# Performance work log

Measured on AMD Instinct MI355X. Metric: run time of the kernel, lower is better.

## Reference

```python
import jax, jax.numpy as jnp
import numpy as np

B, T = 64, 500
N_EX, N_SK = 10000, 100
H, K = 128, 32


def setup_inputs() -> dict:
    key = jax.random.key(0)
    ks = jax.random.split(key, 32)
    g = lambda i, shape, s=0.05: (jax.random.normal(ks[i], shape, dtype=jnp.float32) * s)
    inp = {
        's_data': jax.random.randint(ks[0], (B, T), 0, N_SK),
        'a_data': jax.random.randint(ks[1], (B, T), 0, 2),
        'e_data': jax.random.randint(ks[2], (B, T), 0, N_EX),
        'at_data': jax.random.randint(ks[3], (B, T), 0, 100),
        'q_matrix': (jax.random.uniform(ks[4], (N_EX + 1, N_SK + 1)) < 0.05).astype(jnp.float32),
        's_embed_w': g(5, (N_SK + 1, H)),
        'a_embed_w': g(6, (2, H)),
        'e_embed_w': g(7, (N_EX + 1, H)),
        'W1': g(8, (H, 2 * H)), 'b1': jnp.zeros((H,), jnp.float32),
        'W2': g(9, (H, 3 * H)), 'b2': jnp.zeros((H,), jnp.float32),
        'W3': g(10, (H, 2 * H)), 'b3': jnp.zeros((H,), jnp.float32),
        'key_matrix': g(11, (K, H)),
        'gru_w_ih': g(12, (3 * H, H)), 'gru_w_hh': g(13, (3 * H, H)),
        'gru_b_ih': jnp.zeros((3 * H,), jnp.float32), 'gru_b_hh': jnp.zeros((3 * H,), jnp.float32),
        'Wg': g(14, (H, 2 * H)), 'bg': jnp.zeros((H,), jnp.float32),
        'Wgg': g(15, (H, 2 * H)), 'bgg': jnp.zeros((H,), jnp.float32),
        'Wf': g(16, (H, 2 * H)), 'bf': jnp.zeros((H,), jnp.float32),
        'Wp': g(17, (1, 3 * H)), 'bp': jnp.zeros((1,), jnp.float32),
        'Wp1': g(18, (1, 3 * H)), 'bp1': jnp.zeros((1,), jnp.float32),
        'h0': g(19, (H,)),           # xavier init of GRU initial state (shared across batch)
        'm0': g(20, (K, H)),         # xavier init of memory h_pre (shared across batch)
    }
    return inp


def reference(s_data, a_data, e_data, at_data, q_matrix, s_embed_w, a_embed_w, e_embed_w,
              W1, b1, W2, b2, W3, b3, key_matrix, gru_w_ih, gru_w_hh, gru_b_ih, gru_b_hh,
              Wg, bg, Wgg, bgg, Wf, bf, Wp, bp, Wp1, bp1, h0, m0):
    # eval mode: dropout = identity
    Bv, Tv = a_data.shape
    lin = lambda x, W, b: x @ W.T + b
    # ---- embedding (n_exercise > 0 branch) ----
    rel = q_matrix[e_data]                              # [B,T,S+1]
    ssum = rel.sum(-1, keepdims=True)
    ssum = jnp.where(ssum == 0, 1.0, ssum)
    s_emb = jnp.einsum('bts,sh->bth', rel, s_embed_w) / ssum
    e_emb = e_embed_w[e_data]
    a_emb = a_embed_w[a_data]
    se_data = jax.nn.relu(lin(jnp.concatenate([s_emb, e_emb], -1), W1, b1))
    se_learning = jax.nn.relu(lin(jnp.concatenate([s_emb, e_emb, a_emb], -1), W2, b2))
    e_learning = jax.nn.relu(lin(jnp.concatenate([e_emb, a_emb], -1), W3, b3))
    # ---- GRU over e_learning ----
    gx = jnp.einsum('bth,gh->btg', e_learning, gru_w_ih) + gru_b_ih  # [B,T,3H]
    def gru_step(h, gxt):
        gh = h @ gru_w_hh.T + gru_b_hh
        xr, xz, xn = jnp.split(gxt, 3, -1)
        hr, hz, hn = jnp.split(gh, 3, -1)
        r = jax.nn.sigmoid(xr + hr)
        z = jax.nn.sigmoid(xz + hz)
        n = jnp.tanh(xn + r * hn)
        hn2 = (1 - z) * n + z * h
        return hn2, hn2
    _, gru_out = jax.lax.scan(gru_step, jnp.broadcast_to(h0, (Bv, h0.shape[0])), jnp.swapaxes(gx, 0, 1))
    out = jnp.swapaxes(gru_out, 0, 1)[:, :-1]           # [B,T-1,H]
    # ---- key-value memory scan ----
    Wall = jnp.einsum('bth,kh->btk', se_data, key_matrix)  # attention weights (unnormalized)
    h_pre0 = jnp.broadcast_to(m0, (Bv,) + m0.shape)        # [B,K,H]
    ht0 = jnp.einsum('bk,bkh->bh', Wall[:, 0], h_pre0)
    xs = (jnp.swapaxes(Wall[:, :-1], 0, 1),
          jnp.swapaxes(Wall[:, 1:], 0, 1),
          jnp.swapaxes(se_learning[:, :-1], 0, 1))
    def step(carry, x):
        h_pre, ht_pre = carry
        w, w_next, learning = x
        hl = jnp.concatenate([ht_pre, learning], -1)
        gain = jnp.tanh(hl @ Wg.T + bg)
        gate = jax.nn.sigmoid(hl @ Wgg.T + bgg)
        LG = gate * gain                                  # [B,H]
        LG_t = w[:, :, None] * LG[:, None, :]             # [B,K,H] write
        gam = jax.nn.sigmoid(jnp.concatenate([h_pre, jnp.broadcast_to(LG[:, None, :], h_pre.shape)], -1) @ Wf.T + bf)
        h = gam * h_pre + LG_t
        ht = jnp.einsum('bk,bkh->bh', w_next, h)          # read at t+1
        return (h, ht), ht
    _, hts = jax.lax.scan(step, (h_pre0, ht0), xs)
    out1 = jnp.swapaxes(hts, 0, 1)                        # [B,T-1,H]
    sg = jax.lax.stop_gradient
    res = jax.nn.sigmoid(jnp.concatenate([out, sg(out1), e_emb[:, 1:]], -1) @ Wp.T + bp)[..., 0]
    res1 = jax.nn.sigmoid(jnp.concatenate([sg(out), out1, se_data[:, 1:]], -1) @ Wp1.T + bp1)[..., 0]
    pred = jnp.zeros((Bv, Tv), res.dtype).at[:, 1:].set(res * res1)
    return pred
```

## Files before the change

### kernel.cpp

```cpp
#include <hip/hip_runtime.h>

#define TT 500
typedef __attribute__((ext_vector_type(8))) short short8v;
typedef __attribute__((ext_vector_type(4))) short short4v;
typedef __attribute__((ext_vector_type(4))) float float4v;
typedef unsigned short ushort;

__device__ __forceinline__ ushort f2bf(float f) {
  union { float f; unsigned u; } v; v.f = f;
  unsigned r = v.u + 0x7FFFu + ((v.u >> 16) & 1u);
  return (ushort)(r >> 16);
}
__device__ __forceinline__ ushort f2bfr(float f) {
  union { float f; unsigned u; } v; v.f = f;
  return (ushort)((v.u + 0x8000u) >> 16);
}
__device__ __forceinline__ float bf2f(ushort u) {
  union { unsigned u; float f; } v; v.u = ((unsigned)u) << 16;
  return v.f;
}
__device__ __forceinline__ float sigm(float x) {
  return __builtin_amdgcn_rcpf(1.f + __builtin_amdgcn_exp2f(-1.44269504088896341f * x));
}
__device__ __forceinline__ float tanh_f(float x) {
  return 1.f - 2.f * __builtin_amdgcn_rcpf(1.f + __builtin_amdgcn_exp2f(2.88539008177792682f * x));
}
__device__ __forceinline__ void bar_lds() {
  asm volatile("s_waitcnt lgkmcnt(0)\ns_barrier" ::: "memory");
}
template <int CTRL>
__device__ __forceinline__ float dppadd(float v) {
  int a = __builtin_amdgcn_update_dpp(0, __builtin_bit_cast(int, v), CTRL, 0xF, 0xF, true);
  return v + __builtin_bit_cast(float, a);
}
__device__ __forceinline__ float rsum16(float v) {
  v = dppadd<0xB1>(v);
  v = dppadd<0x4E>(v);
  v = dppadd<0x141>(v);
  v = dppadd<0x140>(v);
  return v;
}
__device__ __forceinline__ void wait_flag(int* f) {
  while (__hip_atomic_load(f, __ATOMIC_RELAXED, __HIP_MEMORY_SCOPE_AGENT) == 0)
    __builtin_amdgcn_s_sleep(8);
  __builtin_amdgcn_fence(__ATOMIC_ACQUIRE, "agent");
}
#define MFMA __builtin_amdgcn_mfma_f32_16x16x32_bf16

__global__ __launch_bounds__(256) void conv_k(
    const float* __restrict__ W1, const float* __restrict__ W2,
    const float* __restrict__ W3, const float* __restrict__ Wih,
    const float* __restrict__ key, const float* __restrict__ Wg,
    const float* __restrict__ Wgg, ushort* __restrict__ wts)
{
  int idx = blockIdx.x * 256 + threadIdx.x;
  if (idx >= 200704) return;
  float v;
  if (idx < 32768)       v = W1[idx];
  else if (idx < 81920)  v = W2[idx - 32768];
  else if (idx < 114688) v = W3[idx - 81920];
  else if (idx < 163840) v = Wih[idx - 114688];
  else if (idx < 167936) v = key[idx - 163840];
  else {
    int j = idx - 167936, o = j >> 7, k = j & 127;
    v = (o < 128) ? Wg[o * 256 + 128 + k] : Wgg[(o - 128) * 256 + 128 + k];
  }
  wts[idx] = f2bf(v);
}

#define XS 424
#define SS 648

__global__ __launch_bounds__(512, 2) void mega_k(
    const int* __restrict__ a_data, const int* __restrict__ e_data,
    const float* __restrict__ qm, const float* __restrict__ semb,
    const float* __restrict__ aemb, const float* __restrict__ eemb,
    const float* __restrict__ b1, const float* __restrict__ b2,
    const float* __restrict__ b3, const float* __restrict__ bih,
    const float* __restrict__ bg, const float* __restrict__ bgg,
    const float* __restrict__ Wp, const float* __restrict__ bp,
    const float* __restrict__ Wp1, const float* __restrict__ bp1,
    const ushort* __restrict__ wts,
    const float* __restrict__ Wf, const float* __restrict__ bf_,
    const float* __restrict__ Wg, const float* __restrict__ Wgg,
    const float* __restrict__ Whh, const float* __restrict__ bhh,
    const float* __restrict__ h0v, const float* __restrict__ m0,
    ushort* __restrict__ gxb, ushort* __restrict__ xgx,
    float* __restrict__ wallb, float* __restrict__ c1b, float* __restrict__ c2b,
    ushort* __restrict__ htsm, ushort* __restrict__ htsg,
    int* __restrict__ flags)
{
  __shared__ __align__(16) ushort pool[27136];
  const int tid = threadIdx.x;
  const int w = tid >> 6, l = tid & 63, jj = l & 15, seg = l >> 4;
  const int n0 = w * 16 + seg * 4;

  if (blockIdx.x < 64) {
    __builtin_amdgcn_s_setprio(3);
    const int b = blockIdx.x;
    ushort* h_bf = pool;
    ushort* htb  = pool + 4096;
    ushort* LGb  = pool + 4224;

    short8v afrA[4], aggA[4], aggB[4], alg[4];
#pragma unroll
    for (int ks = 0; ks < 4; ++ks) {
      const float* sA = Wf  + (w * 16 + jj) * 256 + ks * 32 + seg * 8;
      const float* sB = Wg  + (w * 16 + jj) * 256 + ks * 32 + seg * 8;
      const float* sC = Wgg + (w * 16 + jj) * 256 + ks * 32 + seg * 8;
      const float* sD = Wf  + (w * 16 + jj) * 256 + 128 + ks * 32 + seg * 8;
      short8v a, bb, c, d;
#pragma unroll
      for (int j = 0; j < 8; ++j) {
        a[j] = (short)f2bf(sA[j]); bb[j] = (short)f2bf(sB[j]);
        c[j] = (short)f2bf(sC[j]); d[j] = (short)f2bf(sD[j]);
      }
      afrA[ks] = a; aggA[ks] = bb; aggB[ks] = c; alg[ks] = d;
    }
    const float4v bf4 = *(const float4v*)(bf_ + n0);

    float hreg[2][4];
#pragma unroll
    for (int nt = 0; nt < 2; ++nt) {
      int k = nt * 16 + jj;
      float4v m = *(const float4v*)(m0 + k * 128 + n0);
#pragma unroll
      for (int r = 0; r < 4; ++r) hreg[nt][r] = m[r];
      int p = ((n0 >> 3) + k) & 15;
      short4v pk;
#pragma unroll
      for (int r = 0; r < 4; ++r) pk[r] = (short)f2bf(hreg[nt][r]);
      *(short4v*)(h_bf + k * 128 + p * 8 + (n0 & 7)) = pk;
    }
    wait_flag(flags + b);
    const float* wl = wallb + (size_t)b * TT * 32;
    const ushort* xgp = xgx + (size_t)b * TT * 256;
    float wv0 = wl[jj], wv1 = wl[16 + jj];
    float wn0 = wl[32 + jj], wn1 = wl[48 + jj];
    short4v xcg  = *(const short4v*)(xgp + n0);
    short4v xcgg = *(const short4v*)(xgp + 128 + n0);
    short4v xng  = *(const short4v*)(xgp + 256 + n0);
    short4v xngg = *(const short4v*)(xgp + 384 + n0);
    {
      float4v htp;
#pragma unroll
      for (int r = 0; r < 4; ++r)
        htp[r] = rsum16(wv0 * hreg[0][r] + wv1 * hreg[1][r]);
      if (jj == 0) {
        short4v hp;
#pragma unroll
        for (int r = 0; r < 4; ++r) hp[r] = (short)f2bf(htp[r]);
        *(short4v*)(htb + n0) = hp;
      }
    }
    __syncthreads();

    for (int t = 0; t < TT - 1; ++t) {
      int tw = (t + 2 <= TT - 1) ? (t + 2) : (TT - 1);
      if ((tw & 31) == 0) wait_flag(flags + (tw >> 5) * 64 + b);
      float wf0 = wl[tw * 32 + jj], wf1 = wl[tw * 32 + 16 + jj];
      short4v xfg  = *(const short4v*)(xgp + (size_t)tw * 256 + n0);
      short4v xfgg = *(const short4v*)(xgp + (size_t)tw * 256 + 128 + n0);

      short8v hb[4];
#pragma unroll
      for (int ks = 0; ks < 4; ++ks)
        hb[ks] = *(short8v*)(htb + ks * 32 + seg * 8);

      float4v xg4, xgg4;
#pragma unroll
      for (int r = 0; r < 4; ++r) { xg4[r] = bf2f((ushort)xcg[r]); xgg4[r] = bf2f((ushort)xcgg[r]); }
      float4v dg0 = xg4, dg1 = {0,0,0,0}, gg0 = xgg4, gg1 = {0,0,0,0};
      dg0 = MFMA(aggA[0], hb[0], dg0, 0, 0, 0);
      dg0 = MFMA(aggA[1], hb[1], dg0, 0, 0, 0);
      dg1 = MFMA(aggA[2], hb[2], dg1, 0, 0, 0);
      dg1 = MFMA(aggA[3], hb[3], dg1, 0, 0, 0);
      gg0 = MFMA(aggB[0], hb[0], gg0, 0, 0, 0);
      gg0 = MFMA(aggB[1], hb[1], gg0, 0, 0, 0);
      gg1 = MFMA(aggB[2], hb[2], gg1, 0, 0, 0);
      gg1 = MFMA(aggB[3], hb[3], gg1, 0, 0, 0);

      float lgv[4];
#pragma unroll
      for (int r = 0; r < 4; ++r)
        lgv[r] = tanh_f(dg0[r] + dg1[r]) * sigm(gg0[r] + gg1[r]);
      if (jj == 0) {
        short4v lp;
#pragma unroll
        for (int r = 0; r < 4; ++r) lp[r] = (short)f2bfr(lgv[r]);
        *(short4v*)(LGb + n0) = lp;
      }

      short8v bv0[4], bv1[4];
#pragma unroll
      for (int ks = 0; ks < 4; ++ks) {
        int g = ks * 4 + seg;
        bv0[ks] = *(short8v*)(h_bf + jj * 128 + ((g + jj) & 15) * 8);
        bv1[ks] = *(short8v*)(h_bf + (16 + jj) * 128 + ((g + 16 + jj) & 15) * 8);
      }
      float4v a0A = {0,0,0,0}, a0B = {0,0,0,0}, a1A = {0,0,0,0}, a1B = {0,0,0,0};
      a0A = MFMA(afrA[0], bv0[0], a0A, 0, 0, 0);
      a0A = MFMA(afrA[1], bv0[1], a0A, 0, 0, 0);
      a0B = MFMA(afrA[2], bv0[2], a0B, 0, 0, 0);
      a0B = MFMA(afrA[3], bv0[3], a0B, 0, 0, 0);
      a1A = MFMA(afrA[0], bv1[0], a1A, 0, 0, 0);
      a1A = MFMA(afrA[1], bv1[1], a1A, 0, 0, 0);
      a1B = MFMA(afrA[2], bv1[2], a1B, 0, 0, 0);
      a1B = MFMA(afrA[3], bv1[3], a1B, 0, 0, 0);
      bar_lds();

      short8v lb[4];
#pragma unroll
      for (int ks = 0; ks < 4; ++ks)
        lb[ks] = *(short8v*)(LGb + ks * 32 + seg * 8);
      float4v dl0 = bf4, dl1 = {0,0,0,0};
      dl0 = MFMA(alg[0], lb[0], dl0, 0, 0, 0);
      dl0 = MFMA(alg[1], lb[1], dl0, 0, 0, 0);
      dl1 = MFMA(alg[2], lb[2], dl1, 0, 0, 0);
      dl1 = MFMA(alg[3], lb[3], dl1, 0, 0, 0);

      float4v htp = {0,0,0,0};
#pragma unroll
      for (int nt = 0; nt < 2; ++nt) {
        float wvv = nt ? wv1 : wv0;
        float wnn = nt ? wn1 : wn0;
#pragma unroll
        for (int r = 0; r < 4; ++r) {
          float a = nt ? (a1A[r] + a1B[r]) : (a0A[r] + a0B[r]);
          float gam = sigm(a + dl0[r] + dl1[r]);
          float hn = fmaf(gam, hreg[nt][r], wvv * lgv[r]);
          hreg[nt][r] = hn;
          htp[r] = fmaf(wnn, hn, htp[r]);
        }
        int k = nt * 16 + jj;
        int p = ((n0 >> 3) + k) & 15;
        short4v pk;
#pragma unroll
        for (int r = 0; r < 4; ++r) pk[r] = (short)f2bfr(hreg[nt][r]);
        *(short4v*)(h_bf + k * 128 + p * 8 + (n0 & 7)) = pk;
      }
#pragma unroll
      for (int r = 0; r < 4; ++r) htp[r] = rsum16(htp[r]);
      if (jj == 0) {
        short4v hp;
#pragma unroll
        for (int r = 0; r < 4; ++r) hp[r] = (short)f2bfr(htp[r]);
        *(short4v*)(htb + n0) = hp;
        *(short4v*)(htsm + ((size_t)b * TT + t) * 128 + n0) = hp;
      }
      wv0 = wn0; wv1 = wn1; wn0 = wf0; wn1 = wf1;
      xcg = xng; xcgg = xngg; xng = xfg; xngg = xfgg;
      bar_lds();
    }
  } else if (blockIdx.x < 128) {
    __builtin_amdgcn_s_setprio(3);
    const int b = blockIdx.x - 64;
    ushort* hb2 = pool;

    short8v wfr[3][4];
    float4v bfr[3];
#pragma unroll
    for (int i = 0; i < 3; ++i) {
      int Mt = w + i * 8;
#pragma unroll
      for (int ks = 0; ks < 4; ++ks) {
        const float* src = Whh + (Mt * 16 + jj) * 128 + ks * 32 + seg * 8;
        short8v tv;
#pragma unroll
        for (int j = 0; j < 8; ++j) tv[j] = (short)f2bf(src[j]);
        wfr[i][ks] = tv;
      }
      bfr[i] = *(const float4v*)(bhh + Mt * 16 + seg * 4);
    }
    float4v hj4 = *(const float4v*)(h0v + n0);
    if (jj == 0) {
      short4v hp;
#pragma unroll
      for (int r = 0; r < 4; ++r) hp[r] = (short)f2bf(hj4[r]);
      *(short4v*)(hb2 + n0) = hp;
    }
    wait_flag(flags + b);
    const ushort* gpb = gxb + (size_t)b * TT * 384;
    short4v xr_c = *(const short4v*)(gpb + n0);
    short4v xz_c = *(const short4v*)(gpb + 128 + n0);
    short4v xn_c = *(const short4v*)(gpb + 256 + n0);
    short4v xr_n = *(const short4v*)(gpb + 384 + n0);
    short4v xz_n = *(const short4v*)(gpb + 512 + n0);
    short4v xn_n = *(const short4v*)(gpb + 640 + n0);
    __syncthreads();

    for (int t = 0; t < TT - 1; ++t) {
      int tf = (t + 2 < TT - 1) ? (t + 2) : (TT - 2);
      if ((tf & 31) == 0) wait_flag(flags + (tf >> 5) * 64 + b);
      const ushort* gf = gpb + (size_t)tf * 384;
      short4v xr_f = *(const short4v*)(gf + n0);
      short4v xz_f = *(const short4v*)(gf + 128 + n0);
      short4v xn_f = *(const short4v*)(gf + 256 + n0);

      const ushort* hsrc = hb2 + (t & 1) * 128;
      short8v bfrg[4];
#pragma unroll
      for (int ks = 0; ks < 4; ++ks)
        bfrg[ks] = *(short8v*)(hsrc + ks * 32 + seg * 8);

      float4v a0A = bfr[0], a1A = bfr[1], a2A = bfr[2];
      float4v a0B = {0,0,0,0}, a1B = {0,0,0,0}, a2B = {0,0,0,0};
      a0A = MFMA(wfr[0][0], bfrg[0], a0A, 0, 0, 0);
      a0A = MFMA(wfr[0][1], bfrg[1], a0A, 0, 0, 0);
      a0B = MFMA(wfr[0][2], bfrg[2], a0B, 0, 0, 0);
      a0B = MFMA(wfr[0][3], bfrg[3], a0B, 0, 0, 0);
      a1A = MFMA(wfr[1][0], bfrg[0], a1A, 0, 0, 0);
      a1A = MFMA(wfr[1][1], bfrg[1], a1A, 0, 0, 0);
      a1B = MFMA(wfr[1][2], bfrg[2], a1B, 0, 0, 0);
      a1B = MFMA(wfr[1][3], bfrg[3], a1B, 0, 0, 0);
      a2A = MFMA(wfr[2][0], bfrg[0], a2A, 0, 0, 0);
      a2A = MFMA(wfr[2][1], bfrg[1], a2A, 0, 0, 0);
      a2B = MFMA(wfr[2][2], bfrg[2], a2B, 0, 0, 0);
      a2B = MFMA(wfr[2][3], bfrg[3], a2B, 0, 0, 0);

      ushort* hdst = hb2 + ((t + 1) & 1) * 128;
      short4v hp;
#pragma unroll
      for (int r = 0; r < 4; ++r) {
        float rr = sigm(bf2f((ushort)xr_c[r]) + a0A[r] + a0B[r]);
        float zz = sigm(bf2f((ushort)xz_c[r]) + a1A[r] + a1B[r]);
        float nn = tanh_f(bf2f((ushort)xn_c[r]) + rr * (a2A[r] + a2B[r]));
        hj4[r] = fmaf(1.f - zz, nn, zz * hj4[r]);
        hp[r] = (short)f2bfr(hj4[r]);
      }
      if (jj == 0) {
        *(short4v*)(hdst + n0) = hp;
        *(short4v*)(htsg + ((size_t)b * TT + t) * 128 + n0) = hp;
      }
      xr_c = xr_n; xz_c = xz_n; xn_c = xn_n;
      xr_n = xr_f; xz_n = xz_f; xn_n = xn_f;
      bar_lds();
    }
  } else {
    __builtin_amdgcn_s_setprio(0);
    const int gi = blockIdx.x - 128;
    const int chunk = gi >> 6, b = gi & 63;
    const int t0 = chunk * 32;
    const int NT = (TT - t0 < 32) ? (TT - t0) : 32;
    ushort* Xl = pool;
    ushort* Yl = pool + 13568;
    ushort* St = pool;
    const ushort* w1b  = wts;
    const ushort* w2b  = wts + 32768;
    const ushort* w3b  = wts + 81920;
    const ushort* wihb = wts + 114688;
    const ushort* keyb = wts + 163840;
    const ushort* wgb  = wts + 167936;

    {
      const int tok = tid >> 4, l16 = tid & 15;
      const int tsrc = (tok < NT) ? tok : (NT - 1);
      const int gt = b * TT + t0 + tsrc;
      const int e = e_data[gt], a = a_data[gt];
      const float* qrow = qm + (size_t)e * 101;
      float qv[7];
#pragma unroll
      for (int i = 0; i < 7; ++i) {
        int s = l16 + 16 * i;
        qv[i] = (s < 101) ? qrow[s] : 0.f;
      }
      const float* sbase = semb + l16 * 8;
      float4v acc0 = {0,0,0,0}, acc1 = {0,0,0,0};
      float cnt = 0.f;
#pragma unroll
      for (int i = 0; i < 7; ++i) {
        unsigned long long bal = __ballot(qv[i] != 0.f);
        unsigned m = (unsigned)((bal >> (tid & 48)) & 0xFFFFull);
        cnt += (float)__popc(m);
        while (m) {
          int s = 16 * i + __builtin_ctz(m);
          m &= m - 1;
          acc0 += *(const float4v*)(sbase + s * 128);
          acc1 += *(const float4v*)(sbase + s * 128 + 4);
        }
      }
      float inv = 1.f / fmaxf(cnt, 1.f);
      ushort* xr = Xl + tok * XS + l16 * 8;
#pragma unroll
      for (int r = 0; r < 4; ++r) { xr[r] = f2bf(acc0[r] * inv); xr[4 + r] = f2bf(acc1[r] * inv); }
      const float* ee = eemb + (size_t)e * 128 + l16 * 8;
      const float* ae = aemb + a * 128 + l16 * 8;
#pragma unroll
      for (int r = 0; r < 8; ++r) { xr[128 + r] = f2bf(ee[r]); xr[256 + r] = f2bf(ae[r]); }
    }
    __syncthreads();

    if (tid < 32) {
      int tau = tid;
      if (tau < NT) {
        const ushort* xr = Xl + tau * XS + 128;
        const float* wv = Wp + 256;
        float a0 = bp[0], a1 = 0.f, a2 = 0.f, a3 = 0.f;
        for (int j = 0; j < 128; j += 4) {
          a0 = fmaf(wv[j],     bf2f(xr[j]),     a0);
          a1 = fmaf(wv[j + 1], bf2f(xr[j + 1]), a1);
          a2 = fmaf(wv[j + 2], bf2f(xr[j + 2]), a2);
          a3 = fmaf(wv[j + 3], bf2f(xr[j + 3]), a3);
        }
        c1b[b * TT + t0 + tau] = (a0 + a1) + (a2 + a3);
      }
    }

    short8v axA[12], axB[12];
#pragma unroll
    for (int i = 0; i < 12; ++i) {
      axA[i] = *(short8v*)(Xl + jj * XS + i * 32 + seg * 8);
      axB[i] = *(short8v*)(Xl + (16 + jj) * XS + i * 32 + seg * 8);
    }

    for (int T = w; T < 24; T += 8) {
      float4v dA = {0,0,0,0}, dB = {0,0,0,0};
      float bv;
      if (T < 8) {
        const ushort* Bp = w1b + (T * 16 + jj) * 256 + seg * 8;
        bv = b1[T * 16 + jj];
#pragma unroll
        for (int k = 0; k < 8; ++k) {
          short8v bw = *(const short8v*)(Bp + k * 32);
          dA = MFMA(axA[k], bw, dA, 0, 0, 0);
          dB = MFMA(axB[k], bw, dB, 0, 0, 0);
        }
      } else if (T < 16) {
        const ushort* Bp = w2b + ((T - 8) * 16 + jj) * 384 + seg * 8;
        bv = b2[(T - 8) * 16 + jj];
#pragma unroll
        for (int k = 0; k < 12; ++k) {
          short8v bw = *(const short8v*)(Bp + k * 32);
          dA = MFMA(axA[k], bw, dA, 0, 0, 0);
          dB = MFMA(axB[k], bw, dB, 0, 0, 0);
        }
      } else {
        const ushort* Bp = w3b + ((T - 16) * 16 + jj) * 256 + seg * 8;
        bv = b3[(T - 16) * 16 + jj];
#pragma unroll
        for (int k = 0; k < 8; ++k) {
          short8v bw = *(const short8v*)(Bp + k * 32);
          dA = MFMA(axA[4 + k], bw, dA, 0, 0, 0);
          dB = MFMA(axB[4 + k], bw, dB, 0, 0, 0);
        }
      }
#pragma unroll
      for (int r = 0; r < 4; ++r) {
        float yA = dA[r] + bv, yB = dB[r] + bv;
        Yl[(seg * 4 + r) * XS + T * 16 + jj]      = f2bf(yA > 0.f ? yA : 0.f);
        Yl[(16 + seg * 4 + r) * XS + T * 16 + jj] = f2bf(yB > 0.f ? yB : 0.f);
      }
    }
    __syncthreads();

    short8v ayA[12], ayB[12];
#pragma unroll
    for (int i = 0; i < 12; ++i) {
      ayA[i] = *(short8v*)(Yl + jj * XS + i * 32 + seg * 8);
      ayB[i] = *(short8v*)(Yl + (16 + jj) * XS + i * 32 + seg * 8);
    }
    if (tid >= 32 && tid < 64) {
      int tau = tid - 32;
      if (tau < NT) {
        const ushort* xr = Yl + tau * XS;
        const float* wv = Wp1 + 256;
        float a0 = bp1[0], a1 = 0.f, a2 = 0.f, a3 = 0.f;
        for (int j = 0; j < 128; j += 4) {
          a0 = fmaf(wv[j],     bf2f(xr[j]),     a0);
          a1 = fmaf(wv[j + 1], bf2f(xr[j + 1]), a1);
          a2 = fmaf(wv[j + 2], bf2f(xr[j + 2]), a2);
          a3 = fmaf(wv[j + 3], bf2f(xr[j + 3]), a3);
        }
        c2b[b * TT + t0 + tau] = (a0 + a1) + (a2 + a3);
      }
    }
    __syncthreads();

    for (int T = w; T < 42; T += 8) {
      const ushort* Bp; int ai;
      if (T < 24)      { Bp = wihb + (T * 16 + jj) * 128 + seg * 8;        ai = 8; }
      else if (T < 40) { Bp = wgb  + ((T - 24) * 16 + jj) * 128 + seg * 8; ai = 4; }
      else             { Bp = keyb + ((T - 40) * 16 + jj) * 128 + seg * 8; ai = 0; }
      float4v dA = {0,0,0,0}, dB = {0,0,0,0};
#pragma unroll
      for (int k = 0; k < 4; ++k) {
        short8v bw = *(const short8v*)(Bp + k * 32);
        dA = MFMA(ayA[ai + k], bw, dA, 0, 0, 0);
        dB = MFMA(ayB[ai + k], bw, dB, 0, 0, 0);
      }
      if (T < 40) {
        float bv = (T < 24) ? bih[T * 16 + jj]
                 : (T < 32) ? bg[(T - 24) * 16 + jj] : bgg[(T - 32) * 16 + jj];
        int col = (T < 24) ? (T * 16 + jj) : (384 + (T - 24) * 16 + jj);
#pragma unroll
        for (int r = 0; r < 4; ++r) {
          St[(seg * 4 + r) * SS + col]      = f2bf(dA[r] + bv);
          St[(16 + seg * 4 + r) * SS + col] = f2bf(dB[r] + bv);
        }
      } else {
#pragma unroll
        for (int r = 0; r < 4; ++r) {
          int tokA = seg * 4 + r, tokB = 16 + seg * 4 + r;
          if (tokA < NT)
            wallb[((size_t)(b * TT + t0 + tokA)) * 32 + (T - 40) * 16 + jj] = dA[r];
          if (tokB < NT)
            wallb[((size_t)(b * TT + t0 + tokB)) * 32 + (T - 40) * 16 + jj] = dB[r];
        }
      }
    }
    __syncthreads();

    {
      const int tok = tid >> 4, sg = tid & 15;
      if (tok < NT) {
        size_t gt = (size_t)b * TT + t0 + tok;
#pragma unroll
        for (int p = 0; p < 3; ++p)
          *(short8v*)(gxb + gt * 384 + sg * 24 + p * 8) = *(short8v*)(St + tok * SS + sg * 24 + p * 8);
#pragma unroll
        for (int p = 0; p < 2; ++p)
          *(short8v*)(xgx + gt * 256 + sg * 16 + p * 8) = *(short8v*)(St + tok * SS + 384 + sg * 16 + p * 8);
      }
    }
    __syncthreads();
    if (tid == 0)
      __hip_atomic_store(flags + chunk * 64 + b, 1, __ATOMIC_RELEASE, __HIP_MEMORY_SCOPE_AGENT);
  }
}

__global__ __launch_bounds__(256) void combine_k(
    const ushort* __restrict__ htsg, const ushort* __restrict__ htsm,
    const float* __restrict__ c1b, const float* __restrict__ c2b,
    const float* __restrict__ Wp, const float* __restrict__ Wp1,
    float* __restrict__ out)
{
  const int b = blockIdx.x >> 2, q = blockIdx.x & 3;
  const int tid = threadIdx.x;
  const int wv = tid >> 6, l = tid & 63, slot = l >> 4, e = l & 15;
  float wpg[8], wpm[8], vpg[8], vpm[8];
#pragma unroll
  for (int r = 0; r < 8; ++r) {
    wpg[r] = Wp[e * 8 + r];  wpm[r] = Wp[128 + e * 8 + r];
    vpg[r] = Wp1[e * 8 + r]; vpm[r] = Wp1[128 + e * 8 + r];
  }
  if (q == 0 && tid == 0) out[(size_t)b * TT] = 0.f;
  const int tbeg = q * 125;
  const int tend = (tbeg + 125 < TT - 1) ? (tbeg + 125) : (TT - 1);
  for (int tau = tbeg + wv * 4 + slot; tau < tend; tau += 16) {
    size_t base = ((size_t)b * TT + tau) * 128;
    short8v hg = *(const short8v*)(htsg + base + e * 8);
    short8v hm = *(const short8v*)(htsm + base + e * 8);
    float qa = 0.f, qb = 0.f;
#pragma unroll
    for (int r = 0; r < 8; ++r) {
      float g = bf2f((ushort)hg[r]), m = bf2f((ushort)hm[r]);
      qa = fmaf(g, wpg[r], fmaf(m, wpm[r], qa));
      qb = fmaf(g, vpg[r], fmaf(m, vpm[r], qb));
    }
    qa = rsum16(qa);
    qb = rsum16(qb);
    if (e == 0) {
      size_t idx = (size_t)b * TT + tau + 1;
      out[idx] = sigm(qa + c1b[idx]) * sigm(qb + c2b[idx]);
    }
  }
}

extern "C" void kernel_launch(void* const* d_in, const int* in_sizes, int n_in,
                              void* d_out, int out_size, void* d_ws, size_t ws_size,
                              hipStream_t stream) {
  (void)in_sizes; (void)n_in; (void)out_size; (void)ws_size;
  const int* a_data = (const int*)d_in[1];
  const int* e_data = (const int*)d_in[2];
  const float* qm   = (const float*)d_in[4];
  const float* semb = (const float*)d_in[5];
  const float* aemb = (const float*)d_in[6];
  const float* eemb = (const float*)d_in[7];
  const float* W1 = (const float*)d_in[8];   const float* b1 = (const float*)d_in[9];
  const float* W2 = (const float*)d_in[10];  const float* b2 = (const float*)d_in[11];
  const float* W3 = (const float*)d_in[12];  const float* b3 = (const float*)d_in[13];
  const float* key = (const float*)d_in[14];
  const float* Wih = (const float*)d_in[15]; const float* Whh = (const float*)d_in[16];
  const float* bih = (const float*)d_in[17]; const float* bhh = (const float*)d_in[18];
  const float* Wg  = (const float*)d_in[19]; const float* bg  = (const float*)d_in[20];
  const float* Wgg = (const float*)d_in[21]; const float* bgg = (const float*)d_in[22];
  const float* Wf  = (const float*)d_in[23]; const float* bf_ = (const float*)d_in[24];
  const float* Wp  = (const float*)d_in[25]; const float* bp  = (const float*)d_in[26];
  const float* Wp1 = (const float*)d_in[27]; const float* bp1 = (const float*)d_in[28];
  const float* h0v = (const float*)d_in[29]; const float* m0  = (const float*)d_in[30];

  char* ws = (char*)d_ws;
  ushort* gxb  = (ushort*)(ws + 0);
  ushort* xgx  = (ushort*)(ws + 24576000);
  float* wallb = (float*)(ws + 40960000);
  ushort* htsm = (ushort*)(ws + 45056000);
  ushort* htsg = (ushort*)(ws + 53248000);
  float* c1b   = (float*)(ws + 61440000);
  float* c2b   = (float*)(ws + 61568000);
  ushort* wts  = (ushort*)(ws + 61696000);
  int* flags   = (int*)(ws + 62097408);
  float* out = (float*)d_out;

  hipMemsetAsync(flags, 0, 1024 * sizeof(int), stream);
  conv_k<<<dim3(784), dim3(256), 0, stream>>>(W1, W2, W3, Wih, key, Wg, Wgg, wts);
  mega_k<<<dim3(1152), dim3(512), 0, stream>>>(
      a_data, e_data, qm, semb, aemb, eemb, b1, b2, b3, bih, bg, bgg,
      Wp, bp, Wp1, bp1, wts, Wf, bf_, Wg, Wgg, Whh, bhh, h0v, m0,
      gxb, xgx, wallb, c1b, c2b, htsm, htsg, flags);
  combine_k<<<dim3(256), dim3(256), 0, stream>>>(
      htsg, htsm, c1b, c2b, Wp, Wp1, out);
}
```

Baseline: 833.4 us.

## Split memory-recurrence block into gain-gate warps and forget-gate warps

The per-batch memory-update block is split by role. Four waves compute the LG gain/gate MFMAs and publish LG through LDS in both bf16 and fp32. The other four waves compute the Wf forget-gate MFMAs against the memory state and do the state update, each wave covering twice as many columns. The aim is to overlap the LG computation with the h_pre matmul, but each wave now does double work per step and the LG result crosses an LDS barrier. This changes the critical-path length of the serial recurrence.

```diff
diff --git a/kernel.cpp b/kernel.cpp
--- a/kernel.cpp
+++ b/kernel.cpp
@@ -101,156 +101,222 @@
     ushort* h_bf = pool;
     ushort* htb  = pool + 4096;
     ushort* LGb  = pool + 4224;
-
-    short8v afrA[4], aggA[4], aggB[4], alg[4];
-#pragma unroll
-    for (int ks = 0; ks < 4; ++ks) {
-      const float* sA = Wf  + (w * 16 + jj) * 256 + ks * 32 + seg * 8;
-      const float* sB = Wg  + (w * 16 + jj) * 256 + ks * 32 + seg * 8;
-      const float* sC = Wgg + (w * 16 + jj) * 256 + ks * 32 + seg * 8;
-      const float* sD = Wf  + (w * 16 + jj) * 256 + 128 + ks * 32 + seg * 8;
-      short8v a, bb, c, d;
-#pragma unroll
-      for (int j = 0; j < 8; ++j) {
-        a[j] = (short)f2bf(sA[j]); bb[j] = (short)f2bf(sB[j]);
-        c[j] = (short)f2bf(sC[j]); d[j] = (short)f2bf(sD[j]);
-      }
-      afrA[ks] = a; aggA[ks] = bb; aggB[ks] = c; alg[ks] = d;
-    }
-    const float4v bf4 = *(const float4v*)(bf_ + n0);
-
-    float hreg[2][4];
-#pragma unroll
-    for (int nt = 0; nt < 2; ++nt) {
-      int k = nt * 16 + jj;
-      float4v m = *(const float4v*)(m0 + k * 128 + n0);
-#pragma unroll
-      for (int r = 0; r < 4; ++r) hreg[nt][r] = m[r];
-      int p = ((n0 >> 3) + k) & 15;
-      short4v pk;
-#pragma unroll
-      for (int r = 0; r < 4; ++r) pk[r] = (short)f2bf(hreg[nt][r]);
-      *(short4v*)(h_bf + k * 128 + p * 8 + (n0 & 7)) = pk;
-    }
-    wait_flag(flags + b);
-    const float* wl = wallb + (size_t)b * TT * 32;
-    const ushort* xgp = xgx + (size_t)b * TT * 256;
-    float wv0 = wl[jj], wv1 = wl[16 + jj];
-    float wn0 = wl[32 + jj], wn1 = wl[48 + jj];
-    short4v xcg  = *(const short4v*)(xgp + n0);
-    short4v xcgg = *(const short4v*)(xgp + 128 + n0);
-    short4v xng  = *(const short4v*)(xgp + 256 + n0);
-    short4v xngg = *(const short4v*)(xgp + 384 + n0);
-    {
-      float4v htp;
-#pragma unroll
-      for (int r = 0; r < 4; ++r)
-        htp[r] = rsum16(wv0 * hreg[0][r] + wv1 * hreg[1][r]);
-      if (jj == 0) {
-        short4v hp;
-#pragma unroll
-        for (int r = 0; r < 4; ++r) hp[r] = (short)f2bf(htp[r]);
-        *(short4v*)(htb + n0) = hp;
-      }
-    }
-    __syncthreads();
-
-    for (int t = 0; t < TT - 1; ++t) {
-      int tw = (t + 2 <= TT - 1) ? (t + 2) : (TT - 1);
-      if ((tw & 31) == 0) wait_flag(flags + (tw >> 5) * 64 + b);
-      float wf0 = wl[tw * 32 + jj], wf1 = wl[tw * 32 + 16 + jj];
-      short4v xfg  = *(const short4v*)(xgp + (size_t)tw * 256 + n0);
-      short4v xfgg = *(const short4v*)(xgp + (size_t)tw * 256 + 128 + n0);
-
-      short8v hb[4];
-#pragma unroll
-      for (int ks = 0; ks < 4; ++ks)
-        hb[ks] = *(short8v*)(htb + ks * 32 + seg * 8);
-
-      float4v xg4, xgg4;
-#pragma unroll
-      for (int r = 0; r < 4; ++r) { xg4[r] = bf2f((ushort)xcg[r]); xgg4[r] = bf2f((ushort)xcgg[r]); }
-      float4v dg0 = xg4, dg1 = {0,0,0,0}, gg0 = xgg4, gg1 = {0,0,0,0};
-      dg0 = MFMA(aggA[0], hb[0], dg0, 0, 0, 0);
-      dg0 = MFMA(aggA[1], hb[1], dg0, 0, 0, 0);
-      dg1 = MFMA(aggA[2], hb[2], dg1, 0, 0, 0);
-      dg1 = MFMA(aggA[3], hb[3], dg1, 0, 0, 0);
-      gg0 = MFMA(aggB[0], hb[0], gg0, 0, 0, 0);
-      gg0 = MFMA(aggB[1], hb[1], gg0, 0, 0, 0);
-      gg1 = MFMA(aggB[2], hb[2], gg1, 0, 0, 0);
-      gg1 = MFMA(aggB[3], hb[3], gg1, 0, 0, 0);
-
-      float lgv[4];
-#pragma unroll
-      for (int r = 0; r < 4; ++r)
-        lgv[r] = tanh_f(dg0[r] + dg1[r]) * sigm(gg0[r] + gg1[r]);
-      if (jj == 0) {
-        short4v lp;
-#pragma unroll
-        for (int r = 0; r < 4; ++r) lp[r] = (short)f2bfr(lgv[r]);
-        *(short4v*)(LGb + n0) = lp;
-      }
-
-      short8v bv0[4], bv1[4];
-#pragma unroll
-      for (int ks = 0; ks < 4; ++ks) {
-        int g = ks * 4 + seg;
-        bv0[ks] = *(short8v*)(h_bf + jj * 128 + ((g + jj) & 15) * 8);
-        bv1[ks] = *(short8v*)(h_bf + (16 + jj) * 128 + ((g + 16 + jj) & 15) * 8);
-      }
-      float4v a0A = {0,0,0,0}, a0B = {0,0,0,0}, a1A = {0,0,0,0}, a1B = {0,0,0,0};
-      a0A = MFMA(afrA[0], bv0[0], a0A, 0, 0, 0);
-      a0A = MFMA(afrA[1], bv0[1], a0A, 0, 0, 0);
-      a0B = MFMA(afrA[2], bv0[2], a0B, 0, 0, 0);
-      a0B = MFMA(afrA[3], bv0[3], a0B, 0, 0, 0);
-      a1A = MFMA(afrA[0], bv1[0], a1A, 0, 0, 0);
-      a1A = MFMA(afrA[1], bv1[1], a1A, 0, 0, 0);
-      a1B = MFMA(afrA[2], bv1[2], a1B, 0, 0, 0);
-      a1B = MFMA(afrA[3], bv1[3], a1B, 0, 0, 0);
-      bar_lds();
-
-      short8v lb[4];
-#pragma unroll
-      for (int ks = 0; ks < 4; ++ks)
-        lb[ks] = *(short8v*)(LGb + ks * 32 + seg * 8);
-      float4v dl0 = bf4, dl1 = {0,0,0,0};
-      dl0 = MFMA(alg[0], lb[0], dl0, 0, 0, 0);
-      dl0 = MFMA(alg[1], lb[1], dl0, 0, 0, 0);
-      dl1 = MFMA(alg[2], lb[2], dl1, 0, 0, 0);
-      dl1 = MFMA(alg[3], lb[3], dl1, 0, 0, 0);
-
-      float4v htp = {0,0,0,0};
-#pragma unroll
-      for (int nt = 0; nt < 2; ++nt) {
-        float wvv = nt ? wv1 : wv0;
-        float wnn = nt ? wn1 : wn0;
-#pragma unroll
-        for (int r = 0; r < 4; ++r) {
-          float a = nt ? (a1A[r] + a1B[r]) : (a0A[r] + a0B[r]);
-          float gam = sigm(a + dl0[r] + dl1[r]);
-          float hn = fmaf(gam, hreg[nt][r], wvv * lgv[r]);
-          hreg[nt][r] = hn;
-          htp[r] = fmaf(wnn, hn, htp[r]);
-        }
-        int k = nt * 16 + jj;
-        int p = ((n0 >> 3) + k) & 15;
-        short4v pk;
-#pragma unroll
-        for (int r = 0; r < 4; ++r) pk[r] = (short)f2bfr(hreg[nt][r]);
-        *(short4v*)(h_bf + k * 128 + p * 8 + (n0 & 7)) = pk;
-      }
-#pragma unroll
-      for (int r = 0; r < 4; ++r) htp[r] = rsum16(htp[r]);
-      if (jj == 0) {
-        short4v hp;
-#pragma unroll
-        for (int r = 0; r < 4; ++r) hp[r] = (short)f2bfr(htp[r]);
-        *(short4v*)(htb + n0) = hp;
-        *(short4v*)(htsm + ((size_t)b * TT + t) * 128 + n0) = hp;
-      }
-      wv0 = wn0; wv1 = wn1; wn0 = wf0; wn1 = wf1;
-      xcg = xng; xcgg = xngg; xng = xfg; xngg = xfgg;
-      bar_lds();
+    float*  LGf  = (float*)(pool + 4352);
+
+    if (w < 4) {
+      const int v4 = w;
+      short8v afrA[2][4], alg[2][4];
+      float4v bf4[2];
+#pragma unroll
+      for (int s = 0; s < 2; ++s) {
+        const int rb = v4 * 32 + s * 16;
+#pragma unroll
+        for (int ks = 0; ks < 4; ++ks) {
+          const float* sA = Wf + (rb + jj) * 256 + ks * 32 + seg * 8;
+          const float* sD = Wf + (rb + jj) * 256 + 128 + ks * 32 + seg * 8;
+          short8v a, d;
+#pragma unroll
+          for (int j = 0; j < 8; ++j) { a[j] = (short)f2bf(sA[j]); d[j] = (short)f2bf(sD[j]); }
+          afrA[s][ks] = a; alg[s][ks] = d;
+        }
+        bf4[s] = *(const float4v*)(bf_ + rb + seg * 4);
+      }
+
+      float hreg[2][2][4];
+#pragma unroll
+      for (int s = 0; s < 2; ++s) {
+        const int col0 = v4 * 32 + s * 16 + seg * 4;
+#pragma unroll
+        for (int nt = 0; nt < 2; ++nt) {
+          int k = nt * 16 + jj;
+          float4v m = *(const float4v*)(m0 + k * 128 + col0);
+#pragma unroll
+          for (int r = 0; r < 4; ++r) hreg[s][nt][r] = m[r];
+          int p = ((col0 >> 3) + k) & 15;
+          short4v pk;
+#pragma unroll
+          for (int r = 0; r < 4; ++r) pk[r] = (short)f2bf(hreg[s][nt][r]);
+          *(short4v*)(h_bf + k * 128 + p * 8 + (col0 & 7)) = pk;
+        }
+      }
+      wait_flag(flags + b);
+      const float* wl = wallb + (size_t)b * TT * 32;
+      float wv0 = wl[jj], wv1 = wl[16 + jj];
+      float wn0 = wl[32 + jj], wn1 = wl[48 + jj];
+#pragma unroll
+      for (int s = 0; s < 2; ++s) {
+        const int col0 = v4 * 32 + s * 16 + seg * 4;
+        float4v htp;
+#pragma unroll
+        for (int r = 0; r < 4; ++r)
+          htp[r] = rsum16(wv0 * hreg[s][0][r] + wv1 * hreg[s][1][r]);
+        if (jj == 0) {
+          short4v hp;
+#pragma unroll
+          for (int r = 0; r < 4; ++r) hp[r] = (short)f2bf(htp[r]);
+          *(short4v*)(htb + col0) = hp;
+        }
+      }
+      __syncthreads();
+
+      for (int t = 0; t < TT - 1; ++t) {
+        int tw = (t + 2 <= TT - 1) ? (t + 2) : (TT - 1);
+        if ((tw & 31) == 0) wait_flag(flags + (tw >> 5) * 64 + b);
+        float wf0 = wl[tw * 32 + jj], wf1 = wl[tw * 32 + 16 + jj];
+
+        short8v bv0[4], bv1[4];
+#pragma unroll
+        for (int ks = 0; ks < 4; ++ks) {
+          int g = ks * 4 + seg;
+          bv0[ks] = *(short8v*)(h_bf + jj * 128 + ((g + jj) & 15) * 8);
+          bv1[ks] = *(short8v*)(h_bf + (16 + jj) * 128 + ((g + 16 + jj) & 15) * 8);
+        }
+        float4v a0A[2], a0B[2], a1A[2], a1B[2];
+#pragma unroll
+        for (int s = 0; s < 2; ++s) {
+          float4v z = {0, 0, 0, 0};
+          a0A[s] = z; a0B[s] = z; a1A[s] = z; a1B[s] = z;
+          a0A[s] = MFMA(afrA[s][0], bv0[0], a0A[s], 0, 0, 0);
+          a0A[s] = MFMA(afrA[s][1], bv0[1], a0A[s], 0, 0, 0);
+          a0B[s] = MFMA(afrA[s][2], bv0[2], a0B[s], 0, 0, 0);
+          a0B[s] = MFMA(afrA[s][3], bv0[3], a0B[s], 0, 0, 0);
+          a1A[s] = MFMA(afrA[s][0], bv1[0], a1A[s], 0, 0, 0);
+          a1A[s] = MFMA(afrA[s][1], bv1[1], a1A[s], 0, 0, 0);
+          a1B[s] = MFMA(afrA[s][2], bv1[2], a1B[s], 0, 0, 0);
+          a1B[s] = MFMA(afrA[s][3], bv1[3], a1B[s], 0, 0, 0);
+        }
+        bar_lds();
+
+        short8v lb[4];
+#pragma unroll
+        for (int ks = 0; ks < 4; ++ks)
+          lb[ks] = *(short8v*)(LGb + ks * 32 + seg * 8);
+        float4v lgf[2];
+#pragma unroll
+        for (int s = 0; s < 2; ++s)
+          lgf[s] = *(const float4v*)(LGf + v4 * 32 + s * 16 + seg * 4);
+
+#pragma unroll
+        for (int s = 0; s < 2; ++s) {
+          float4v dl0 = bf4[s], dl1 = {0, 0, 0, 0};
+          dl0 = MFMA(alg[s][0], lb[0], dl0, 0, 0, 0);
+          dl0 = MFMA(alg[s][1], lb[1], dl0, 0, 0, 0);
+          dl1 = MFMA(alg[s][2], lb[2], dl1, 0, 0, 0);
+          dl1 = MFMA(alg[s][3], lb[3], dl1, 0, 0, 0);
+
+          const int col0 = v4 * 32 + s * 16 + seg * 4;
+          float4v htp = {0, 0, 0, 0};
+#pragma unroll
+          for (int nt = 0; nt < 2; ++nt) {
+            float wvv = nt ? wv1 : wv0;
+            float wnn = nt ? wn1 : wn0;
+#pragma unroll
+            for (int r = 0; r < 4; ++r) {
+              float a = nt ? (a1A[s][r] + a1B[s][r]) : (a0A[s][r] + a0B[s][r]);
+              float gam = sigm(a + dl0[r] + dl1[r]);
+              float hn = fmaf(gam, hreg[s][nt][r], wvv * lgf[s][r]);
+              hreg[s][nt][r] = hn;
+              htp[r] = fmaf(wnn, hn, htp[r]);
+            }
+            int k = nt * 16 + jj;
+            int p = ((col0 >> 3) + k) & 15;
+            short4v pk;
+#pragma unroll
+            for (int r = 0; r < 4; ++r) pk[r] = (short)f2bfr(hreg[s][nt][r]);
+            *(short4v*)(h_bf + k * 128 + p * 8 + (col0 & 7)) = pk;
+          }
+#pragma unroll
+          for (int r = 0; r < 4; ++r) htp[r] = rsum16(htp[r]);
+          if (jj == 0) {
+            short4v hp;
+#pragma unroll
+            for (int r = 0; r < 4; ++r) hp[r] = (short)f2bfr(htp[r]);
+            *(short4v*)(htb + col0) = hp;
+            *(short4v*)(htsm + ((size_t)b * TT + t) * 128 + col0) = hp;
+          }
+        }
+        wv0 = wn0; wv1 = wn1; wn0 = wf0; wn1 = wf1;
+        bar_lds();
+      }
+    } else {
+      const int u = w - 4;
+      short8v aggA[2][4], aggB[2][4];
+#pragma unroll
+      for (int s = 0; s < 2; ++s) {
+        const int rb = u * 32 + s * 16;
+#pragma unroll
+        for (int ks = 0; ks < 4; ++ks) {
+          const float* sB = Wg  + (rb + jj) * 256 + ks * 32 + seg * 8;
+          const float* sC = Wgg + (rb + jj) * 256 + ks * 32 + seg * 8;
+          short8v bb, c;
+#pragma unroll
+          for (int j = 0; j < 8; ++j) { bb[j] = (short)f2bf(sB[j]); c[j] = (short)f2bf(sC[j]); }
+          aggA[s][ks] = bb; aggB[s][ks] = c;
+        }
+      }
+      wait_flag(flags + b);
+      const ushort* xgp = xgx + (size_t)b * TT * 256;
+      short4v xcg[2], xcgg[2], xng[2], xngg[2];
+#pragma unroll
+      for (int s = 0; s < 2; ++s) {
+        const int col0 = u * 32 + s * 16 + seg * 4;
+        xcg[s]  = *(const short4v*)(xgp + col0);
+        xcgg[s] = *(const short4v*)(xgp + 128 + col0);
+        xng[s]  = *(const short4v*)(xgp + 256 + col0);
+        xngg[s] = *(const short4v*)(xgp + 384 + col0);
+      }
+      __syncthreads();
+
+      for (int t = 0; t < TT - 1; ++t) {
+        int tw = (t + 2 <= TT - 1) ? (t + 2) : (TT - 1);
+        if ((tw & 31) == 0) wait_flag(flags + (tw >> 5) * 64 + b);
+        short4v xfg[2], xfgg[2];
+#pragma unroll
+        for (int s = 0; s < 2; ++s) {
+          const int col0 = u * 32 + s * 16 + seg * 4;
+          xfg[s]  = *(const short4v*)(xgp + (size_t)tw * 256 + col0);
+          xfgg[s] = *(const short4v*)(xgp + (size_t)tw * 256 + 128 + col0);
+        }
+        short8v hb[4];
+#pragma unroll
+        for (int ks = 0; ks < 4; ++ks)
+          hb[ks] = *(short8v*)(htb + ks * 32 + seg * 8);
+
+#pragma unroll
+        for (int s = 0; s < 2; ++s) {
+          float4v xg4, xgg4;
+#pragma unroll
+          for (int r = 0; r < 4; ++r) {
+            xg4[r] = bf2f((ushort)xcg[s][r]);
+            xgg4[r] = bf2f((ushort)xcgg[s][r]);
+          }
+          float4v dg0 = xg4, dg1 = {0, 0, 0, 0}, gg0 = xgg4, gg1 = {0, 0, 0, 0};
+          dg0 = MFMA(aggA[s][0], hb[0], dg0, 0, 0, 0);
+          dg0 = MFMA(aggA[s][1], hb[1], dg0, 0, 0, 0);
+          dg1 = MFMA(aggA[s][2], hb[2], dg1, 0, 0, 0);
+          dg1 = MFMA(aggA[s][3], hb[3], dg1, 0, 0, 0);
+          gg0 = MFMA(aggB[s][0], hb[0], gg0, 0, 0, 0);
+          gg0 = MFMA(aggB[s][1], hb[1], gg0, 0, 0, 0);
+          gg1 = MFMA(aggB[s][2], hb[2], gg1, 0, 0, 0);
+          gg1 = MFMA(aggB[s][3], hb[3], gg1, 0, 0, 0);
+
+          float4v lgvv;
+#pragma unroll
+          for (int r = 0; r < 4; ++r)
+            lgvv[r] = tanh_f(dg0[r] + dg1[r]) * sigm(gg0[r] + gg1[r]);
+          const int col0 = u * 32 + s * 16 + seg * 4;
+          if (jj == 0) {
+            short4v lp;
+#pragma unroll
+            for (int r = 0; r < 4; ++r) lp[r] = (short)f2bfr(lgvv[r]);
+            *(short4v*)(LGb + col0) = lp;
+            *(float4v*)(LGf + col0) = lgvv;
+          }
+          xcg[s] = xng[s]; xcgg[s] = xngg[s]; xng[s] = xfg[s]; xngg[s] = xfgg[s];
+        }
+        bar_lds();
+        bar_lds();
+      }
     }
   } else if (blockIdx.x < 128) {
     __builtin_amdgcn_s_setprio(3);
```

After: 886.6 us. 6.4% more time.

## Pack two batch recurrences per 1024-thread block and widen producer blocks

Applied to the files above, without the earlier changes.

Doubles the block size to 1024 threads. Each memory-recurrence and GRU block now runs two independent batch rows as two 8-wave units, so only 32+32 blocks handle the serial scans. The producer blocks use 16 waves, which halves per-wave tile loops and changes the embedding gather to 32 lanes per token. This aims to free CUs and raise throughput, but the launch bound of 1024 threads at occupancy 4 squeezes the register budget. Block-wide barriers in the recurrence now couple the two units and may slow each step. Barrier semantics (bar_lds) across the two units are unchanged, and the flag-based producer/consumer indexing is assumed to still line up.

```diff
diff --git a/kernel.cpp b/kernel.cpp
--- a/kernel.cpp
+++ b/kernel.cpp
@@ -71,7 +71,7 @@
 #define XS 424
 #define SS 648
 
-__global__ __launch_bounds__(512, 2) void mega_k(
+__global__ __launch_bounds__(1024, 4) void mega_k(
     const int* __restrict__ a_data, const int* __restrict__ e_data,
     const float* __restrict__ qm, const float* __restrict__ semb,
     const float* __restrict__ aemb, const float* __restrict__ eemb,
@@ -93,22 +93,23 @@
   __shared__ __align__(16) ushort pool[27136];
   const int tid = threadIdx.x;
   const int w = tid >> 6, l = tid & 63, jj = l & 15, seg = l >> 4;
-  const int n0 = w * 16 + seg * 4;
-
-  if (blockIdx.x < 64) {
+  const int u8 = w & 7, unit = w >> 3;
+  const int n0 = u8 * 16 + seg * 4;
+
+  if (blockIdx.x < 32) {
     __builtin_amdgcn_s_setprio(3);
-    const int b = blockIdx.x;
-    ushort* h_bf = pool;
-    ushort* htb  = pool + 4096;
-    ushort* LGb  = pool + 4224;
+    const int b = blockIdx.x + unit * 32;
+    ushort* h_bf = pool + unit * 4352;
+    ushort* htb  = h_bf + 4096;
+    ushort* LGb  = h_bf + 4224;
 
     short8v afrA[4], aggA[4], aggB[4], alg[4];
 #pragma unroll
     for (int ks = 0; ks < 4; ++ks) {
-      const float* sA = Wf  + (w * 16 + jj) * 256 + ks * 32 + seg * 8;
-      const float* sB = Wg  + (w * 16 + jj) * 256 + ks * 32 + seg * 8;
-      const float* sC = Wgg + (w * 16 + jj) * 256 + ks * 32 + seg * 8;
-      const float* sD = Wf  + (w * 16 + jj) * 256 + 128 + ks * 32 + seg * 8;
+      const float* sA = Wf  + (u8 * 16 + jj) * 256 + ks * 32 + seg * 8;
+      const float* sB = Wg  + (u8 * 16 + jj) * 256 + ks * 32 + seg * 8;
+      const float* sC = Wgg + (u8 * 16 + jj) * 256 + ks * 32 + seg * 8;
+      const float* sD = Wf  + (u8 * 16 + jj) * 256 + 128 + ks * 32 + seg * 8;
       short8v a, bb, c, d;
 #pragma unroll
       for (int j = 0; j < 8; ++j) {
@@ -252,16 +253,16 @@
       xcg = xng; xcgg = xngg; xng = xfg; xngg = xfgg;
       bar_lds();
     }
-  } else if (blockIdx.x < 128) {
+  } else if (blockIdx.x < 64) {
     __builtin_amdgcn_s_setprio(3);
-    const int b = blockIdx.x - 64;
-    ushort* hb2 = pool;
+    const int b = (blockIdx.x - 32) + unit * 32;
+    ushort* hb2 = pool + unit * 4352;
 
     short8v wfr[3][4];
     float4v bfr[3];
 #pragma unroll
     for (int i = 0; i < 3; ++i) {
-      int Mt = w + i * 8;
+      int Mt = u8 + i * 8;
 #pragma unroll
       for (int ks = 0; ks < 4; ++ks) {
         const float* src = Whh + (Mt * 16 + jj) * 128 + ks * 32 + seg * 8;
@@ -338,7 +339,7 @@
     }
   } else {
     __builtin_amdgcn_s_setprio(0);
-    const int gi = blockIdx.x - 128;
+    const int gi = blockIdx.x - 64;
     const int chunk = gi >> 6, b = gi & 63;
     const int t0 = chunk * 32;
     const int NT = (TT - t0 < 32) ? (TT - t0) : 32;
@@ -353,40 +354,39 @@
     const ushort* wgb  = wts + 167936;
 
     {
-      const int tok = tid >> 4, l16 = tid & 15;
+      const int tok = tid >> 5, l32 = tid & 31;
       const int tsrc = (tok < NT) ? tok : (NT - 1);
       const int gt = b * TT + t0 + tsrc;
       const int e = e_data[gt], a = a_data[gt];
       const float* qrow = qm + (size_t)e * 101;
-      float qv[7];
-#pragma unroll
-      for (int i = 0; i < 7; ++i) {
-        int s = l16 + 16 * i;
+      float qv[4];
+#pragma unroll
+      for (int i = 0; i < 4; ++i) {
+        int s = l32 + 32 * i;
         qv[i] = (s < 101) ? qrow[s] : 0.f;
       }
-      const float* sbase = semb + l16 * 8;
-      float4v acc0 = {0,0,0,0}, acc1 = {0,0,0,0};
+      const float* sbase = semb + l32 * 4;
+      float4v acc = {0,0,0,0};
       float cnt = 0.f;
 #pragma unroll
-      for (int i = 0; i < 7; ++i) {
+      for (int i = 0; i < 4; ++i) {
         unsigned long long bal = __ballot(qv[i] != 0.f);
-        unsigned m = (unsigned)((bal >> (tid & 48)) & 0xFFFFull);
+        unsigned m = (unsigned)(bal >> (tid & 32));
         cnt += (float)__popc(m);
         while (m) {
-          int s = 16 * i + __builtin_ctz(m);
+          int s = 32 * i + __builtin_ctz(m);
           m &= m - 1;
-          acc0 += *(const float4v*)(sbase + s * 128);
-          acc1 += *(const float4v*)(sbase + s * 128 + 4);
+          acc += *(const float4v*)(sbase + s * 128);
         }
       }
       float inv = 1.f / fmaxf(cnt, 1.f);
-      ushort* xr = Xl + tok * XS + l16 * 8;
-#pragma unroll
-      for (int r = 0; r < 4; ++r) { xr[r] = f2bf(acc0[r] * inv); xr[4 + r] = f2bf(acc1[r] * inv); }
-      const float* ee = eemb + (size_t)e * 128 + l16 * 8;
-      const float* ae = aemb + a * 128 + l16 * 8;
-#pragma unroll
-      for (int r = 0; r < 8; ++r) { xr[128 + r] = f2bf(ee[r]); xr[256 + r] = f2bf(ae[r]); }
+      ushort* xr = Xl + tok * XS + l32 * 4;
+#pragma unroll
+      for (int r = 0; r < 4; ++r) xr[r] = f2bf(acc[r] * inv);
+      const float* ee = eemb + (size_t)e * 128 + l32 * 4;
+      const float* ae = aemb + a * 128 + l32 * 4;
+#pragma unroll
+      for (int r = 0; r < 4; ++r) { xr[128 + r] = f2bf(ee[r]); xr[256 + r] = f2bf(ae[r]); }
     }
     __syncthreads();
 
@@ -413,7 +413,7 @@
       axB[i] = *(short8v*)(Xl + (16 + jj) * XS + i * 32 + seg * 8);
     }
 
-    for (int T = w; T < 24; T += 8) {
+    for (int T = w; T < 24; T += 16) {
       float4v dA = {0,0,0,0}, dB = {0,0,0,0};
       float bv;
       if (T < 8) {
@@ -476,7 +476,7 @@
     }
     __syncthreads();
 
-    for (int T = w; T < 42; T += 8) {
+    for (int T = w; T < 42; T += 16) {
       const ushort* Bp; int ai;
       if (T < 24)      { Bp = wihb + (T * 16 + jj) * 128 + seg * 8;        ai = 8; }
       else if (T < 40) { Bp = wgb  + ((T - 24) * 16 + jj) * 128 + seg * 8; ai = 4; }
@@ -603,7 +603,7 @@
 
   hipMemsetAsync(flags, 0, 1024 * sizeof(int), stream);
   conv_k<<<dim3(784), dim3(256), 0, stream>>>(W1, W2, W3, Wih, key, Wg, Wgg, wts);
-  mega_k<<<dim3(1152), dim3(512), 0, stream>>>(
+  mega_k<<<dim3(1088), dim3(1024), 0, stream>>>(
       a_data, e_data, qm, semb, aemb, eemb, b1, b2, b3, bih, bg, bgg,
       Wp, bp, Wp1, bp1, wts, Wf, bf_, Wg, Wgg, Whh, bhh, h0v, m0,
       gxb, xgx, wallb, c1b, c2b, htsm, htsg, flags);
```

Result: slower. 2.418 ms (+190.1%).
